# Kernel optimization log

Hardware: AMD Instinct MI355X
Metric: run time of the kernel (lower is better)

Reference implementation:

```python
import jax, jax.numpy as jnp
import numpy as np

BATCH, SEQLEN, D_MODEL, D_STATE, D_FF = 16, 8192, 256, 256, 1024
RMIN, RMAX, MAX_PHASE = 0.0, 1.0, 2.0 * np.pi


def setup_inputs() -> dict:
    key = jax.random.key(0)
    ks = jax.random.split(key, 12)
    x = jax.random.normal(ks[0], (BATCH, SEQLEN, D_MODEL), jnp.float32)
    # LRU stable exponential parameterization (Orvieto et al.)
    u1 = jax.random.uniform(ks[1], (D_STATE,), jnp.float32)
    u2 = jax.random.uniform(ks[2], (D_STATE,), jnp.float32)
    nu_log = jnp.log(-0.5 * jnp.log(u1 * (RMAX**2 - RMIN**2) + RMIN**2))
    theta_log = jnp.log(MAX_PHASE * u2)
    lam_abs = jnp.exp(-jnp.exp(nu_log))
    gamma_log = 0.5 * jnp.log(1.0 - lam_abs**2)
    B_re = jax.random.normal(ks[3], (D_STATE, D_MODEL), jnp.float32) / np.sqrt(2.0 * D_MODEL)
    B_im = jax.random.normal(ks[4], (D_STATE, D_MODEL), jnp.float32) / np.sqrt(2.0 * D_MODEL)
    C_re = jax.random.normal(ks[5], (D_MODEL, D_STATE), jnp.float32) / np.sqrt(D_STATE)
    C_im = jax.random.normal(ks[6], (D_MODEL, D_STATE), jnp.float32) / np.sqrt(D_STATE)
    D = jax.random.normal(ks[7], (D_MODEL, D_MODEL), jnp.float32) / np.sqrt(D_MODEL)
    W_fc = jax.random.normal(ks[8], (D_MODEL, D_FF), jnp.float32) / np.sqrt(D_MODEL)
    b_fc = jnp.zeros((D_FF,), jnp.float32)
    W_proj = jax.random.normal(ks[9], (D_FF, D_MODEL), jnp.float32) / np.sqrt(D_FF)
    b_proj = jnp.zeros((D_MODEL,), jnp.float32)
    return dict(x=x, nu_log=nu_log, theta_log=theta_log, gamma_log=gamma_log,
                B_re=B_re, B_im=B_im, C_re=C_re, C_im=C_im, D=D,
                W_fc=W_fc, b_fc=b_fc, W_proj=W_proj, b_proj=b_proj)


def _lru_scan(x, nu_log, theta_log, gamma_log, B_re, B_im, C_re, C_im, D):
    # diagonal complex recurrence: s_t = lam * s_{t-1} + gamma * B @ u_t ; y_t = Re(C s_t) + D u_t
    lam = jnp.exp(-jnp.exp(nu_log)) * jnp.exp(1j * jnp.exp(theta_log))      # (S,) complex
    Bn = (B_re + 1j * B_im) * jnp.exp(gamma_log)[:, None]                   # (S, D)
    Bu = jnp.einsum('bld,sd->bls', x + 0j, Bn)                              # (B, L, S) complex
    lam_b = jnp.broadcast_to(lam, Bu.shape)

    def comb(a, b):
        a_l, a_s = a
        b_l, b_s = b
        return a_l * b_l, b_l * a_s + b_s

    _, states = jax.lax.associative_scan(comb, (lam_b, Bu), axis=1)
    C = C_re + 1j * C_im
    return jnp.einsum('bls,os->blo', states, C).real + x @ D.T


def reference(x, nu_log, theta_log, gamma_log, B_re, B_im, C_re, C_im, D,
              W_fc, b_fc, W_proj, b_proj):
    z = _lru_scan(x, nu_log, theta_log, gamma_log, B_re, B_im, C_re, C_im, D)
    # MLP (dropout=0 -> identity)
    h = jax.nn.gelu(z @ W_fc + b_fc, approximate=False)
    z = h @ W_proj + b_proj
    return z + x  # residual
```

## Files before the change

kernel.cpp:

```cpp
#include <hip/hip_runtime.h>
#include <hip/hip_bf16.h>
#include <math.h>

#define B_SZ 16
#define L_SZ 8192
#define DM   256
#define SS   256
#define FF   1024
#define M_SZ (B_SZ * L_SZ)
#define TCH  128
#define NCH  (L_SZ / TCH)

#define BM 128
#define BN 128
#define BK 32

typedef __bf16 bf16x8 __attribute__((ext_vector_type(8)));
typedef float  f32x4  __attribute__((ext_vector_type(4)));

__device__ __forceinline__ void gld_lds16(const __bf16* g, __bf16* l) {
  __builtin_amdgcn_global_load_lds(
      (const __attribute__((address_space(1))) unsigned int*)g,
      (__attribute__((address_space(3))) unsigned int*)l, 16, 0, 0);
}

__device__ __forceinline__ float gelu_exact_fast(float t) {
  const float at = fabsf(t);
  const float a  = at * 0.70710678118654752f;
  const float k  = __builtin_amdgcn_rcpf(fmaf(0.3275911f, a, 1.0f));
  float P = fmaf(1.061405429f, k, -1.453152027f);
  P = fmaf(P, k, 1.421413741f);
  P = fmaf(P, k, -0.284496736f);
  P = fmaf(P, k, 0.254829592f);
  P = P * k;
  const float e = __expf(-a * a);
  const float half_t  = 0.5f * t;
  const float half_at = 0.5f * at;
  return fmaf(-half_at, P * e, half_t + half_at);
}

__global__ void prep_kernel(const float* __restrict__ nu_log, const float* __restrict__ th_log,
                            const float* __restrict__ ga_log,
                            const float* __restrict__ B_re, const float* __restrict__ B_im,
                            const float* __restrict__ C_re, const float* __restrict__ C_im,
                            const float* __restrict__ Dmat,
                            const float* __restrict__ W_fc, const float* __restrict__ W_proj,
                            __bf16* __restrict__ Wb, __bf16* __restrict__ Wz,
                            __bf16* __restrict__ Wfc, __bf16* __restrict__ Wp,
                            float* __restrict__ lam)
{
  const int idx = blockIdx.x * 256 + threadIdx.x;
  if (idx < SS) {
    float la = expf(-expf(nu_log[idx]));
    float th = expf(th_log[idx]);
    lam[2*idx]   = la * cosf(th);
    lam[2*idx+1] = la * sinf(th);
  }
  if (idx < SS*DM) {
    int s = idx >> 8, d = idx & 255;
    float eg = expf(ga_log[s]);
    Wb[(size_t)(2*s)*DM + d]   = (__bf16)(B_re[idx] * eg);
    Wb[(size_t)(2*s+1)*DM + d] = (__bf16)(B_im[idx] * eg);
  }
  if (idx < DM*SS) {
    int o = idx >> 8, s = idx & 255;
    Wz[(size_t)o*768 + 2*s]     = (__bf16)( C_re[idx]);
    Wz[(size_t)o*768 + 2*s + 1] = (__bf16)(-C_im[idx]);
    Wz[(size_t)o*768 + 512 + s] = (__bf16)( Dmat[idx]);
  }
  if (idx < FF*DM) {
    int f = idx >> 8, d = idx & 255;
    Wfc[idx] = (__bf16)(W_fc[(size_t)d*FF + f]);
    int o = idx >> 10, f2 = idx & 1023;
    Wp[idx] = (__bf16)(W_proj[(size_t)f2*DM + o]);
  }
}

__global__ __launch_bounds__(256) void convert_x(const float* __restrict__ x, __bf16* __restrict__ S_all)
{
  const long i = ((long)blockIdx.x * 256 + threadIdx.x) * 4;
  float4 v = *(const float4*)(x + i);
  const long m = i >> 8;
  const int  d = (int)(i & 255);
  union { __bf16 h[4]; uint2 u; } pk;
  pk.h[0] = (__bf16)v.x; pk.h[1] = (__bf16)v.y; pk.h[2] = (__bf16)v.z; pk.h[3] = (__bf16)v.w;
  *(uint2*)(S_all + m*768 + 512 + d) = pk.u;
}

template<int K, int LDA, int LDC, int MODE, int NT>
__global__ __launch_bounds__(256, 2) void gemm_bt(const __bf16* __restrict__ A,
                                                  const __bf16* __restrict__ Bw,
                                                  void* __restrict__ Cout,
                                                  const float* __restrict__ bias,
                                                  const float* __restrict__ resid)
{
  __shared__ __attribute__((aligned(16))) __bf16 sA[2][BM * BK];
  __shared__ __attribute__((aligned(16))) __bf16 sB[2][BN * BK];

  const int tid  = threadIdx.x;
  const int lane = tid & 63;
  const int wave = tid >> 6;
  const int wm = (wave & 1) * 64;
  const int wn = (wave >> 1) * 64;

  constexpr int PER = 16 * NT;
  const int blk = blockIdx.x;
  const int sb  = blk / PER;
  const int rem = blk & (PER - 1);
  const long m0 = (long)((sb << 4) + (rem & 15)) * BM;
  const long n0 = (long)(rem >> 4) * BN;

  f32x4 acc[4][4] = {};

  const int r  = tid >> 2;
  const int c8 = (tid & 3) * 8;
  const __bf16* gA = A  + (m0 + r) * (long)LDA + c8;
  const __bf16* gB = Bw + (n0 + r) * (long)K   + c8;

  const int ar = lane & 15;
  const int ak = (lane >> 4) * 8;

  constexpr int NK = K / BK;

  gld_lds16(gA,                  &sA[0][tid * 8]);
  gld_lds16(gA + 64 * (long)LDA, &sA[0][2048 + tid * 8]);
  gld_lds16(gB,                  &sB[0][tid * 8]);
  gld_lds16(gB + 64 * (long)K,   &sB[0][2048 + tid * 8]);
  gA += BK; gB += BK;
  __syncthreads();

  int cur = 0;
  #pragma unroll 2
  for (int i = 0; i < NK; ++i) {
    if (i + 1 < NK) {
      const int nxt = cur ^ 1;
      gld_lds16(gA,                  &sA[nxt][tid * 8]);
      gld_lds16(gA + 64 * (long)LDA, &sA[nxt][2048 + tid * 8]);
      gld_lds16(gB,                  &sB[nxt][tid * 8]);
      gld_lds16(gB + 64 * (long)K,   &sB[nxt][2048 + tid * 8]);
      gA += BK; gB += BK;
    }

    bf16x8 af[4], bg[4];
    #pragma unroll
    for (int ii = 0; ii < 4; ++ii)
      af[ii] = *(const bf16x8*)&sA[cur][(wm + ii * 16 + ar) * BK + ak];
    #pragma unroll
    for (int j = 0; j < 4; ++j)
      bg[j] = *(const bf16x8*)&sB[cur][(wn + j * 16 + ar) * BK + ak];
    #pragma unroll
    for (int ii = 0; ii < 4; ++ii)
      #pragma unroll
      for (int j = 0; j < 4; ++j)
        acc[ii][j] = __builtin_amdgcn_mfma_f32_16x16x32_bf16(af[ii], bg[j], acc[ii][j], 0, 0, 0);

    __syncthreads();
    cur ^= 1;
  }

  const int col_l = lane & 15;
  const int row_l = (lane >> 4) * 4;
  #pragma unroll
  for (int i = 0; i < 4; ++i) {
    #pragma unroll
    for (int j = 0; j < 4; ++j) {
      const long row = m0 + wm + i * 16 + row_l;
      const long col = n0 + wn + j * 16 + col_l;
      #pragma unroll
      for (int rr = 0; rr < 4; ++rr) {
        const float v = acc[i][j][rr];
        const long idx = (row + rr) * (long)LDC + col;
        if constexpr (MODE == 1) {
          ((__bf16*)Cout)[idx] = (__bf16)v;
        } else if constexpr (MODE == 2) {
          const float t = v + bias[col];
          ((__bf16*)Cout)[idx] = (__bf16)gelu_exact_fast(t);
        } else {
          ((float*)Cout)[idx] = v + bias[col] + resid[idx];
        }
      }
    }
  }
}

#define CSTEP(vr, vi) { float nr_ = fmaf(lr, sr, fmaf(-li, si, (vr))); \
                        float ni_ = fmaf(lr, si, fmaf( li, sr, (vi))); sr = nr_; si = ni_; }

union bupk { unsigned int u; __bf16 h[2]; };

__global__ __launch_bounds__(256) void scan_carry(const __bf16* __restrict__ Bu,
                                                  const float* __restrict__ lam,
                                                  float2* __restrict__ carr)
{
  const int s  = threadIdx.x;
  const int bc = blockIdx.x;
  const float lr = lam[2*s], li = lam[2*s+1];
  const unsigned int* bu = (const unsigned int*)(Bu + (size_t)bc * (TCH * 512)) + s;
  float sr = 0.f, si = 0.f;
  bupk v0, v1, v2, v3;
  v0.u = bu[0]; v1.u = bu[256]; v2.u = bu[512]; v3.u = bu[768];
  for (int t = 0; t < TCH - 4; t += 4) {
    bupk n0, n1, n2, n3;
    n0.u = bu[(t+4)*256]; n1.u = bu[(t+5)*256]; n2.u = bu[(t+6)*256]; n3.u = bu[(t+7)*256];
    CSTEP((float)v0.h[0], (float)v0.h[1]); CSTEP((float)v1.h[0], (float)v1.h[1]);
    CSTEP((float)v2.h[0], (float)v2.h[1]); CSTEP((float)v3.h[0], (float)v3.h[1]);
    v0 = n0; v1 = n1; v2 = n2; v3 = n3;
  }
  CSTEP((float)v0.h[0], (float)v0.h[1]); CSTEP((float)v1.h[0], (float)v1.h[1]);
  CSTEP((float)v2.h[0], (float)v2.h[1]); CSTEP((float)v3.h[0], (float)v3.h[1]);
  carr[(size_t)bc * 256 + s] = make_float2(sr, si);
}

__global__ __launch_bounds__(256) void scan_prefix(const float2* __restrict__ carr,
                                                   const float* __restrict__ lam,
                                                   float2* __restrict__ pre)
{
  const int s = threadIdx.x;
  const int b = blockIdx.x;
  float ar = lam[2*s], ai = lam[2*s+1];
  #pragma unroll
  for (int i = 0; i < 7; ++i) { float nr = ar*ar - ai*ai, ni = 2.f*ar*ai; ar = nr; ai = ni; }
  float pr = 0.f, pi = 0.f;
  for (int c = 0; c < NCH; ++c) {
    const size_t off = (size_t)(b * NCH + c) * 256 + s;
    pre[off] = make_float2(pr, pi);
    float2 cv = carr[off];
    float nr = fmaf(ar, pr, fmaf(-ai, pi, cv.x));
    float ni = fmaf(ar, pi, fmaf( ai, pr, cv.y));
    pr = nr; pi = ni;
  }
}

__global__ __launch_bounds__(256) void scan_apply(const __bf16* __restrict__ Bu,
                                                  const float* __restrict__ lam,
                                                  const float2* __restrict__ pre,
                                                  __bf16* __restrict__ S_all)
{
  const int s  = threadIdx.x;
  const int bc = blockIdx.x;
  const float lr = lam[2*s], li = lam[2*s+1];
  float2 p = pre[(size_t)bc * 256 + s];
  float sr = p.x, si = p.y;
  const unsigned int* bu = (const unsigned int*)(Bu + (size_t)bc * (TCH * 512)) + s;
  __bf16* outp = S_all + (size_t)bc * (TCH * 768) + 2 * s;
  #define APSTEP(v, t) { CSTEP((float)(v).h[0], (float)(v).h[1]); \
    union { __bf16 h[2]; unsigned int u; } pk_; pk_.h[0] = (__bf16)sr; pk_.h[1] = (__bf16)si; \
    *(unsigned int*)(outp + (size_t)(t) * 768) = pk_.u; }
  bupk v0, v1, v2, v3;
  v0.u = bu[0]; v1.u = bu[256]; v2.u = bu[512]; v3.u = bu[768];
  for (int t = 0; t < TCH - 4; t += 4) {
    bupk n0, n1, n2, n3;
    n0.u = bu[(t+4)*256]; n1.u = bu[(t+5)*256]; n2.u = bu[(t+6)*256]; n3.u = bu[(t+7)*256];
    APSTEP(v0, t); APSTEP(v1, t+1); APSTEP(v2, t+2); APSTEP(v3, t+3);
    v0 = n0; v1 = n1; v2 = n2; v3 = n3;
  }
  { const int t = TCH - 4; APSTEP(v0, t); APSTEP(v1, t+1); APSTEP(v2, t+2); APSTEP(v3, t+3); }
  #undef APSTEP
}

extern "C" void kernel_launch(void* const* d_in, const int* in_sizes, int n_in,
                              void* d_out, int out_size, void* d_ws, size_t ws_size,
                              hipStream_t stream)
{
  const float* x      = (const float*)d_in[0];
  const float* nu_log = (const float*)d_in[1];
  const float* th_log = (const float*)d_in[2];
  const float* ga_log = (const float*)d_in[3];
  const float* B_re   = (const float*)d_in[4];
  const float* B_im   = (const float*)d_in[5];
  const float* C_re   = (const float*)d_in[6];
  const float* C_im   = (const float*)d_in[7];
  const float* Dmat   = (const float*)d_in[8];
  const float* W_fc   = (const float*)d_in[9];
  const float* b_fc   = (const float*)d_in[10];
  const float* W_proj = (const float*)d_in[11];
  const float* b_proj = (const float*)d_in[12];

  char* ws = (char*)d_ws;
  __bf16* S_all = (__bf16*)(ws);
  __bf16* Bu    = (__bf16*)(ws + 201326592);
  __bf16* Hbuf  = (__bf16*)(ws + 201326592);
  __bf16* Wb    = (__bf16*)(ws + 469762048);
  __bf16* Wz    = (__bf16*)(ws + 470024192);
  __bf16* Wfc   = (__bf16*)(ws + 470417408);
  __bf16* Wp    = (__bf16*)(ws + 470941696);
  float*  lam   = (float*) (ws + 471465984);
  if (ws_size < 471468032ULL) return;

  char* ob = (char*)d_out;
  __bf16* Zbuf = (__bf16*)ob;
  float2* carr = (float2*)(ob + 67108864);
  float2* pre  = (float2*)(ob + 69206016);

  prep_kernel<<<1024, 256, 0, stream>>>(nu_log, th_log, ga_log, B_re, B_im,
                                        C_re, C_im, Dmat, W_fc, W_proj,
                                        Wb, Wz, Wfc, Wp, lam);
  convert_x<<<M_SZ * DM / (256 * 4), 256, 0, stream>>>(x, S_all);

  gemm_bt<256, 768, 512, 1, 4><<<(M_SZ / BM) * 4, 256, 0, stream>>>(S_all + 512, Wb, Bu, nullptr, nullptr);

  scan_carry <<<B_SZ * NCH, 256, 0, stream>>>(Bu, lam, carr);
  scan_prefix<<<B_SZ,       256, 0, stream>>>(carr, lam, pre);
  scan_apply <<<B_SZ * NCH, 256, 0, stream>>>(Bu, lam, pre, S_all);

  gemm_bt<768, 768, 256, 1, 2><<<(M_SZ / BM) * 2, 256, 0, stream>>>(S_all, Wz, Zbuf, nullptr, nullptr);
  gemm_bt<256, 256, 1024, 2, 8><<<(M_SZ / BM) * 8, 256, 0, stream>>>(Zbuf, Wfc, Hbuf, b_fc, nullptr);
  gemm_bt<1024, 1024, 256, 3, 2><<<(M_SZ / BM) * 2, 256, 0, stream>>>(Hbuf, Wp, d_out, b_proj, x);
}
```

Baseline: 751.1 us.

## Load GEMM B fragments directly to registers and stage epilogue through LDS

The GEMM now loads B-operand fragments straight from global memory into registers, prefetching one k-step ahead, and keeps only the A tile in LDS. This cuts LDS traffic and footprint. The epilogue writes accumulators to a swizzled LDS buffer in two halves, then reads them back row-contiguous so each thread emits wide 16-byte stores, with vectorized bias and residual reads. It adds extra barriers and uncoalesced per-lane global B loads in exchange for coalesced output writes.

```diff
diff --git a/kernel.cpp b/kernel.cpp
--- a/kernel.cpp
+++ b/kernel.cpp
@@ -94,8 +94,7 @@
                                                   const float* __restrict__ bias,
                                                   const float* __restrict__ resid)
 {
-  __shared__ __attribute__((aligned(16))) __bf16 sA[2][BM * BK];
-  __shared__ __attribute__((aligned(16))) __bf16 sB[2][BN * BK];
+  __shared__ __attribute__((aligned(16))) __bf16 smem[16384];
 
   const int tid  = threadIdx.x;
   const int lane = tid & 63;
@@ -114,72 +113,128 @@
 
   const int r  = tid >> 2;
   const int c8 = (tid & 3) * 8;
-  const __bf16* gA = A  + (m0 + r) * (long)LDA + c8;
-  const __bf16* gB = Bw + (n0 + r) * (long)K   + c8;
+  const __bf16* gA = A + (m0 + r) * (long)LDA + c8;
 
   const int ar = lane & 15;
   const int ak = (lane >> 4) * 8;
 
+  const __bf16* gB0 = Bw + (n0 + wn +  0 + ar) * (long)K + ak;
+  const __bf16* gB1 = Bw + (n0 + wn + 16 + ar) * (long)K + ak;
+  const __bf16* gB2 = Bw + (n0 + wn + 32 + ar) * (long)K + ak;
+  const __bf16* gB3 = Bw + (n0 + wn + 48 + ar) * (long)K + ak;
+
   constexpr int NK = K / BK;
 
-  gld_lds16(gA,                  &sA[0][tid * 8]);
-  gld_lds16(gA + 64 * (long)LDA, &sA[0][2048 + tid * 8]);
-  gld_lds16(gB,                  &sB[0][tid * 8]);
-  gld_lds16(gB + 64 * (long)K,   &sB[0][2048 + tid * 8]);
-  gA += BK; gB += BK;
+  gld_lds16(gA,                  &smem[tid * 8]);
+  gld_lds16(gA + 64 * (long)LDA, &smem[2048 + tid * 8]);
+  gA += BK;
+  bf16x8 bg[4], bgN[4];
+  bg[0] = *(const bf16x8*)gB0;
+  bg[1] = *(const bf16x8*)gB1;
+  bg[2] = *(const bf16x8*)gB2;
+  bg[3] = *(const bf16x8*)gB3;
   __syncthreads();
 
   int cur = 0;
   #pragma unroll 2
   for (int i = 0; i < NK; ++i) {
+    const __bf16* sAc = smem + cur * 4096;
     if (i + 1 < NK) {
-      const int nxt = cur ^ 1;
-      gld_lds16(gA,                  &sA[nxt][tid * 8]);
-      gld_lds16(gA + 64 * (long)LDA, &sA[nxt][2048 + tid * 8]);
-      gld_lds16(gB,                  &sB[nxt][tid * 8]);
-      gld_lds16(gB + 64 * (long)K,   &sB[nxt][2048 + tid * 8]);
-      gA += BK; gB += BK;
+      __bf16* sAn = smem + (cur ^ 1) * 4096;
+      gld_lds16(gA,                  &sAn[tid * 8]);
+      gld_lds16(gA + 64 * (long)LDA, &sAn[2048 + tid * 8]);
+      gA += BK;
+      const long ko = (long)(i + 1) * BK;
+      bgN[0] = *(const bf16x8*)(gB0 + ko);
+      bgN[1] = *(const bf16x8*)(gB1 + ko);
+      bgN[2] = *(const bf16x8*)(gB2 + ko);
+      bgN[3] = *(const bf16x8*)(gB3 + ko);
     }
 
-    bf16x8 af[4], bg[4];
+    bf16x8 af[4];
     #pragma unroll
     for (int ii = 0; ii < 4; ++ii)
-      af[ii] = *(const bf16x8*)&sA[cur][(wm + ii * 16 + ar) * BK + ak];
-    #pragma unroll
-    for (int j = 0; j < 4; ++j)
-      bg[j] = *(const bf16x8*)&sB[cur][(wn + j * 16 + ar) * BK + ak];
+      af[ii] = *(const bf16x8*)&sAc[(wm + ii * 16 + ar) * BK + ak];
     #pragma unroll
     for (int ii = 0; ii < 4; ++ii)
       #pragma unroll
       for (int j = 0; j < 4; ++j)
         acc[ii][j] = __builtin_amdgcn_mfma_f32_16x16x32_bf16(af[ii], bg[j], acc[ii][j], 0, 0, 0);
 
+    #pragma unroll
+    for (int j = 0; j < 4; ++j) bg[j] = bgN[j];
     __syncthreads();
     cur ^= 1;
   }
 
+  float* ldsF = (float*)smem;
   const int col_l = lane & 15;
   const int row_l = (lane >> 4) * 4;
+  const int er  = tid >> 2;
+  const int ec0 = (tid & 3) * 32;
+  const int esw = (er & 7) << 2;
+
   #pragma unroll
-  for (int i = 0; i < 4; ++i) {
-    #pragma unroll
-    for (int j = 0; j < 4; ++j) {
-      const long row = m0 + wm + i * 16 + row_l;
-      const long col = n0 + wn + j * 16 + col_l;
+  for (int h = 0; h < 2; ++h) {
+    if (wm == h * 64) {
       #pragma unroll
-      for (int rr = 0; rr < 4; ++rr) {
-        const float v = acc[i][j][rr];
-        const long idx = (row + rr) * (long)LDC + col;
-        if constexpr (MODE == 1) {
-          ((__bf16*)Cout)[idx] = (__bf16)v;
-        } else if constexpr (MODE == 2) {
-          const float t = v + bias[col];
-          ((__bf16*)Cout)[idx] = (__bf16)gelu_exact_fast(t);
-        } else {
-          ((float*)Cout)[idx] = v + bias[col] + resid[idx];
+      for (int i = 0; i < 4; ++i)
+        #pragma unroll
+        for (int j = 0; j < 4; ++j) {
+          const int colb = wn + j * 16 + col_l;
+          #pragma unroll
+          for (int rr = 0; rr < 4; ++rr) {
+            const int rowb = i * 16 + row_l + rr;
+            ldsF[rowb * 128 + (colb ^ ((rowb & 7) << 2))] = acc[i][j][rr];
+          }
+        }
+    }
+    __syncthreads();
+    {
+      const long grow = m0 + h * 64 + er;
+      f32x4 vv[8];
+      #pragma unroll
+      for (int q = 0; q < 8; ++q)
+        vv[q] = *(const f32x4*)&ldsF[er * 128 + ((ec0 + q * 4) ^ esw)];
+
+      if constexpr (MODE == 1) {
+        #pragma unroll
+        for (int q = 0; q < 4; ++q) {
+          union { __bf16 hh[8]; uint4 u; } pk;
+          #pragma unroll
+          for (int e = 0; e < 4; ++e) {
+            pk.hh[e]     = (__bf16)vv[2*q][e];
+            pk.hh[4 + e] = (__bf16)vv[2*q+1][e];
+          }
+          *(uint4*)((__bf16*)Cout + grow * (long)LDC + n0 + ec0 + q * 8) = pk.u;
+        }
+      } else if constexpr (MODE == 2) {
+        #pragma unroll
+        for (int q = 0; q < 4; ++q) {
+          const f32x4 b0 = *(const f32x4*)(bias + n0 + ec0 + q * 8);
+          const f32x4 b1 = *(const f32x4*)(bias + n0 + ec0 + q * 8 + 4);
+          union { __bf16 hh[8]; uint4 u; } pk;
+          #pragma unroll
+          for (int e = 0; e < 4; ++e) {
+            pk.hh[e]     = (__bf16)gelu_exact_fast(vv[2*q][e]   + b0[e]);
+            pk.hh[4 + e] = (__bf16)gelu_exact_fast(vv[2*q+1][e] + b1[e]);
+          }
+          *(uint4*)((__bf16*)Cout + grow * (long)LDC + n0 + ec0 + q * 8) = pk.u;
+        }
+      } else {
+        #pragma unroll
+        for (int q = 0; q < 8; ++q) {
+          const long cidx = grow * (long)LDC + n0 + ec0 + q * 4;
+          const f32x4 rv = *(const f32x4*)(resid + cidx);
+          const f32x4 bv = *(const f32x4*)(bias + n0 + ec0 + q * 4);
+          f32x4 o;
+          #pragma unroll
+          for (int e = 0; e < 4; ++e) o[e] = vv[q][e] + bv[e] + rv[e];
+          *(f32x4*)((float*)Cout + cidx) = o;
         }
       }
     }
+    __syncthreads();
   }
 }
 
```

After: 993.2 us. 1.32x slower.
